# Performance work log

Measured on AMD Instinct MI355X. Metric: run time of the kernel, lower is better.

The kernel has to match this reference:

```python
import jax, jax.numpy as jnp
import numpy as np

D_MODEL = 1024
NUM_HEADS = 16
D_K = D_MODEL // NUM_HEADS


def setup_inputs() -> dict:
    key = jax.random.key(0)
    ks = jax.random.split(key, 9)
    B, S = 2, 2048
    scale = 1.0 / np.sqrt(D_MODEL)
    x = jax.random.normal(ks[0], (B, S, D_MODEL), dtype=jnp.float32)
    Wq = jax.random.normal(ks[1], (D_MODEL, D_MODEL), dtype=jnp.float32) * scale
    Wk = jax.random.normal(ks[2], (D_MODEL, D_MODEL), dtype=jnp.float32) * scale
    Wv = jax.random.normal(ks[3], (D_MODEL, D_MODEL), dtype=jnp.float32) * scale
    Wo = jax.random.normal(ks[4], (D_MODEL, D_MODEL), dtype=jnp.float32) * scale
    bq = jax.random.normal(ks[5], (D_MODEL,), dtype=jnp.float32) * 0.01
    bk = jax.random.normal(ks[6], (D_MODEL,), dtype=jnp.float32) * 0.01
    bv = jax.random.normal(ks[7], (D_MODEL,), dtype=jnp.float32) * 0.01
    bo = jax.random.normal(ks[8], (D_MODEL,), dtype=jnp.float32) * 0.01
    return {"x": x, "Wq": Wq, "bq": bq, "Wk": Wk, "bk": bk,
            "Wv": Wv, "bv": bv, "Wo": Wo, "bo": bo}


def reference(x, Wq, bq, Wk, bk, Wv, bv, Wo, bo):
    B, S, _ = x.shape
    H, Dk = NUM_HEADS, D_K
    # projections -> [B, H, S, Dk]
    def split_heads(t):
        return t.reshape(B, S, H, Dk).transpose(0, 2, 1, 3)
    q = split_heads(x @ Wq + bq)
    k = split_heads(x @ Wk + bk)
    v = split_heads(x @ Wv + bv)
    # full score matrix [B, H, S, S] (faithful to the original non-fused impl)
    scores = jnp.einsum('bhqd,bhkd->bhqk', q, k) / jnp.sqrt(jnp.float32(Dk))
    attn = jax.nn.softmax(scores, axis=-1)
    out = jnp.einsum('bhqk,bhkd->bhqd', attn, v)
    out = out.transpose(0, 2, 1, 3).reshape(B, S, H * Dk)
    return out @ Wo + bo
```

## Files before the change

### kernel.cpp

```cpp
#include <hip/hip_runtime.h>
#include <cstdint>

constexpr int S    = 2048;
constexpr int D    = 1024;
constexpr int NH   = 16;
constexpr int DK   = 64;
constexpr int MTOK = 2 * S;

typedef __bf16 bf16x8 __attribute__((ext_vector_type(8)));
typedef __bf16 bf16x4 __attribute__((ext_vector_type(4)));
typedef float  floatx4 __attribute__((ext_vector_type(4)));

__device__ __forceinline__ void async_cp16(const void* g, void* l) {
    __builtin_amdgcn_global_load_lds(
        (const __attribute__((address_space(1))) uint32_t*)g,
        (__attribute__((address_space(3))) uint32_t*)l, 16, 0, 0);
}

__global__ __launch_bounds__(256) void cvt_prep(
    const float* __restrict__ x, __bf16* __restrict__ xb,
    const float* __restrict__ W0, const float* __restrict__ W1,
    const float* __restrict__ W2, const float* __restrict__ W3,
    __bf16* __restrict__ T0, __bf16* __restrict__ T1,
    __bf16* __restrict__ T2, __bf16* __restrict__ T3)
{
    const int t = threadIdx.x;
    if (blockIdx.z == 4) {
        int blk = blockIdx.y * 16 + blockIdx.x;
        const float4* src = (const float4*)x;
        #pragma unroll
        for (int ii = 0; ii < 16; ++ii) {
            int idx = blk * 4096 + ii * 256 + t;
            float4 v = src[idx];
            bf16x4 o;
            o[0] = (__bf16)v.x; o[1] = (__bf16)v.y; o[2] = (__bf16)v.z; o[3] = (__bf16)v.w;
            *(bf16x4*)&xb[(size_t)idx * 4] = o;
        }
        return;
    }
    const float* W = (blockIdx.z == 0) ? W0 : (blockIdx.z == 1) ? W1 : (blockIdx.z == 2) ? W2 : W3;
    __bf16*      T = (blockIdx.z == 0) ? T0 : (blockIdx.z == 1) ? T1 : (blockIdx.z == 2) ? T2 : T3;
    __shared__ __bf16 tile[64][65];
    const int k0 = blockIdx.y * 64, n0 = blockIdx.x * 64;
    #pragma unroll
    for (int i = 0; i < 4; ++i) {
        int k = (t >> 4) + i * 16;
        int n = (t & 15) * 4;
        float4 v = *(const float4*)&W[(size_t)(k0 + k) * D + n0 + n];
        tile[n + 0][k] = (__bf16)v.x;
        tile[n + 1][k] = (__bf16)v.y;
        tile[n + 2][k] = (__bf16)v.z;
        tile[n + 3][k] = (__bf16)v.w;
    }
    __syncthreads();
    #pragma unroll
    for (int i = 0; i < 4; ++i) {
        int n = (t >> 4) + i * 16;
        int k = (t & 15) * 4;
        bf16x4 o;
        o[0] = tile[n][k]; o[1] = tile[n][k + 1]; o[2] = tile[n][k + 2]; o[3] = tile[n][k + 3];
        *(bf16x4*)&T[(size_t)(n0 + n) * D + k0 + k] = o;
    }
}

constexpr int BM = 128, BK = 64;

template<int JT>
__device__ __forceinline__ void gemm_core(
    const __bf16* __restrict__ A, const __bf16* __restrict__ Bt,
    __bf16* Alds, __bf16* Blds, int m0, int n0, floatx4 (&acc)[4][JT])
{
    const int tid = threadIdx.x;
    const int w = tid >> 6, l = tid & 63;
    const int wm = (w >> 1) * 64, wn = (w & 1) * 16 * JT;
    const int lr = l & 15, lg = l >> 4;

    #pragma unroll
    for (int i = 0; i < 4; ++i)
        #pragma unroll
        for (int j = 0; j < JT; ++j)
            acc[i][j] = (floatx4){0.f, 0.f, 0.f, 0.f};

    for (int k0 = 0; k0 < D; k0 += BK) {
        #pragma unroll
        for (int i = 0; i < 4; ++i) {
            int c = i * 256 + tid, row = c >> 3, g = c & 7;
            async_cp16(&A[(size_t)(m0 + row) * D + k0 + g * 8], &Alds[c * 8]);
        }
        #pragma unroll
        for (int i = 0; i < JT; ++i) {
            int c = i * 256 + tid, row = c >> 3, g = c & 7;
            async_cp16(&Bt[(size_t)(n0 + row) * D + k0 + g * 8], &Blds[c * 8]);
        }
        __syncthreads();
        #pragma unroll
        for (int kk = 0; kk < 2; ++kk) {
            bf16x8 af[4], bfr[JT];
            #pragma unroll
            for (int i = 0; i < 4; ++i)
                af[i] = *(const bf16x8*)&Alds[(wm + i * 16 + lr) * BK + kk * 32 + lg * 8];
            #pragma unroll
            for (int j = 0; j < JT; ++j)
                bfr[j] = *(const bf16x8*)&Blds[(wn + j * 16 + lr) * BK + kk * 32 + lg * 8];
            #pragma unroll
            for (int i = 0; i < 4; ++i)
                #pragma unroll
                for (int j = 0; j < JT; ++j)
                    acc[i][j] = __builtin_amdgcn_mfma_f32_16x16x32_bf16(af[i], bfr[j], acc[i][j], 0, 0, 0);
        }
        __syncthreads();
    }
}

__global__ __launch_bounds__(256, 2) void gemm_qkv(
    const __bf16* __restrict__ xb,
    const __bf16* __restrict__ WqT, const __bf16* __restrict__ WkT, const __bf16* __restrict__ WvT,
    const float* __restrict__ bq, const float* __restrict__ bk, const float* __restrict__ bv,
    __bf16* __restrict__ Qb, __bf16* __restrict__ Kb, __bf16* __restrict__ Vt)
{
    __shared__ __align__(16) __bf16 Alds[BM * BK];
    __shared__ __align__(16) __bf16 Blds[128 * BK];
    const int z = blockIdx.z;
    const __bf16* Bt   = (z == 0) ? WqT : (z == 1) ? WkT : WvT;
    const float*  bias = (z == 0) ? bq : (z == 1) ? bk : bv;
    const float   scale = (z == 0) ? 0.18033688f : 1.0f;
    const int m0 = blockIdx.y * BM, n0 = blockIdx.x * 128;

    floatx4 acc[4][4];
    gemm_core<4>(xb, Bt, Alds, Blds, m0, n0, acc);

    const int tid = threadIdx.x;
    const int w = tid >> 6, l = tid & 63;
    const int wm = (w >> 1) * 64, wn = (w & 1) * 64;
    const int lr = l & 15, lg = l >> 4;

    if (z < 2) {
        __bf16* Out = (z == 0) ? Qb : Kb;
        #pragma unroll
        for (int i = 0; i < 4; ++i)
            #pragma unroll
            for (int j = 0; j < 4; ++j) {
                int n = n0 + wn + j * 16 + lr;
                #pragma unroll
                for (int r = 0; r < 4; ++r) {
                    int m = m0 + wm + i * 16 + lg * 4 + r;
                    float v = (acc[i][j][r] + bias[n]) * scale;
                    size_t off = ((size_t)((m >> 11) * NH + (n >> 6)) * S + (m & (S - 1))) * DK + (n & (DK - 1));
                    Out[off] = (__bf16)v;
                }
            }
    } else {
        #pragma unroll
        for (int i = 0; i < 4; ++i)
            #pragma unroll
            for (int j = 0; j < 4; ++j) {
                int n = n0 + wn + j * 16 + lr;
                int m = m0 + wm + i * 16 + lg * 4;
                float bn = bias[n];
                bf16x4 o;
                #pragma unroll
                for (int r = 0; r < 4; ++r) o[r] = (__bf16)(acc[i][j][r] + bn);
                size_t off = ((size_t)((m >> 11) * NH + (n >> 6)) * DK + (n & (DK - 1))) * S + (m & (S - 1));
                *(bf16x4*)&Vt[off] = o;
            }
    }
}

__global__ __launch_bounds__(256, 2) void gemm_out(
    const __bf16* __restrict__ A, const __bf16* __restrict__ Bt,
    const float* __restrict__ bias, float* __restrict__ Cout)
{
    __shared__ __align__(16) __bf16 Alds[BM * BK];
    __shared__ __align__(16) __bf16 Blds[64 * BK];
    const int m0 = blockIdx.y * BM, n0 = blockIdx.x * 64;

    floatx4 acc[4][2];
    gemm_core<2>(A, Bt, Alds, Blds, m0, n0, acc);

    const int tid = threadIdx.x;
    const int w = tid >> 6, l = tid & 63;
    const int wm = (w >> 1) * 64, wn = (w & 1) * 32;
    const int lr = l & 15, lg = l >> 4;
    #pragma unroll
    for (int i = 0; i < 4; ++i)
        #pragma unroll
        for (int j = 0; j < 2; ++j) {
            int n = n0 + wn + j * 16 + lr;
            #pragma unroll
            for (int r = 0; r < 4; ++r) {
                int m = m0 + wm + i * 16 + lg * 4 + r;
                Cout[(size_t)m * D + n] = acc[i][j][r] + bias[n];
            }
        }
}

constexpr int QT = 128;
constexpr int KT = 64;
constexpr float SOFTMAX_C2 = 14.4269504f;

__global__ __launch_bounds__(256, 2) void attn_mfma(
    const __bf16* __restrict__ Q, const __bf16* __restrict__ K,
    const __bf16* __restrict__ Vt, __bf16* __restrict__ O)
{
    __shared__ __align__(16) __bf16 Klds[2][KT * DK];
    __shared__ __align__(16) __bf16 Vlds[2][DK * KT];
    __shared__ __align__(16) __bf16 Plds[4][32 * 64];

    const int tid = threadIdx.x;
    const int w = tid >> 6, l = tid & 63;
    const int lr = l & 15, lg = l >> 4;
    const int sw = lr & 7;
    const int bh = blockIdx.y;
    const int q0 = blockIdx.x * QT;
    const __bf16* Kbase = K  + (size_t)bh * S * DK;
    const __bf16* Vbase = Vt + (size_t)bh * DK * S;

    bf16x8 qf[2][2];
    {
        const __bf16* qp = Q + ((size_t)bh * S + q0 + w * 32) * DK;
        #pragma unroll
        for (int i = 0; i < 2; ++i)
            #pragma unroll
            for (int kk = 0; kk < 2; ++kk)
                qf[i][kk] = *(const bf16x8*)&qp[(i * 16 + lr) * DK + kk * 32 + lg * 8];
    }
    bf16x8 vones;
    #pragma unroll
    for (int j = 0; j < 8; ++j) vones[j] = (__bf16)1.0f;

    floatx4 acc[4][2];
    #pragma unroll
    for (int jd = 0; jd < 4; ++jd)
        #pragma unroll
        for (int i = 0; i < 2; ++i)
            acc[jd][i] = (floatx4){0.f, 0.f, 0.f, 0.f};
    floatx4 psacc[2];
    psacc[0] = (floatx4){0.f, 0.f, 0.f, 0.f};
    psacc[1] = (floatx4){0.f, 0.f, 0.f, 0.f};

    bf16x8 kreg[2], vreg[2];
    auto gload = [&](int t0) {
        #pragma unroll
        for (int ii = 0; ii < 2; ++ii) {
            int c = ii * 256 + tid, row = c >> 3, g = c & 7;
            kreg[ii] = *(const bf16x8*)&Kbase[(size_t)(t0 + row) * DK + g * 8];
            vreg[ii] = *(const bf16x8*)&Vbase[(size_t)row * S + t0 + g * 8];
        }
    };
    auto lwrite = [&](int buf) {
        #pragma unroll
        for (int ii = 0; ii < 2; ++ii) {
            int c = ii * 256 + tid, row = c >> 3, gs = (c & 7) ^ (row & 7);
            *(bf16x8*)&Klds[buf][row * 64 + gs * 8] = kreg[ii];
            *(bf16x8*)&Vlds[buf][row * 64 + gs * 8] = vreg[ii];
        }
    };

    gload(0);
    lwrite(0);
    gload(KT);

    for (int t0 = 0; t0 < S; t0 += KT) {
        const int cur = (t0 >> 6) & 1;
        __syncthreads();

        floatx4 sa[4][2];
        #pragma unroll
        for (int j = 0; j < 4; ++j)
            #pragma unroll
            for (int i = 0; i < 2; ++i)
                sa[j][i] = (floatx4){0.f, 0.f, 0.f, 0.f};
        #pragma unroll
        for (int kk = 0; kk < 2; ++kk) {
            bf16x8 kf[4];
            #pragma unroll
            for (int j = 0; j < 4; ++j)
                kf[j] = *(const bf16x8*)&Klds[cur][(j * 16 + lr) * DK + (((kk * 4 + lg) ^ sw) * 8)];
            #pragma unroll
            for (int j = 0; j < 4; ++j)
                #pragma unroll
                for (int i = 0; i < 2; ++i)
                    sa[j][i] = __builtin_amdgcn_mfma_f32_16x16x32_bf16(kf[j], qf[i][kk], sa[j][i], 0, 0, 0);
        }

        #pragma unroll
        for (int j = 0; j < 4; ++j)
            #pragma unroll
            for (int i = 0; i < 2; ++i) {
                bf16x4 pb;
                #pragma unroll
                for (int r = 0; r < 4; ++r)
                    pb[r] = (__bf16)__builtin_amdgcn_exp2f(sa[j][i][r] - SOFTMAX_C2);
                int gsw = (j * 2 + (lg >> 1)) ^ sw;
                *(bf16x4*)&Plds[w][(i * 16 + lr) * 64 + gsw * 8 + (lg & 1) * 4] = pb;
            }

        #pragma unroll
        for (int kk = 0; kk < 2; ++kk) {
            bf16x8 vf[4], pf[2];
            #pragma unroll
            for (int i = 0; i < 2; ++i) {
                int gsw = (kk * 4 + lg) ^ sw;
                pf[i] = *(const bf16x8*)&Plds[w][(i * 16 + lr) * 64 + gsw * 8];
            }
            #pragma unroll
            for (int jd = 0; jd < 4; ++jd)
                vf[jd] = *(const bf16x8*)&Vlds[cur][(jd * 16 + lr) * KT + (((kk * 4 + lg) ^ sw) * 8)];
            #pragma unroll
            for (int jd = 0; jd < 4; ++jd)
                #pragma unroll
                for (int i = 0; i < 2; ++i)
                    acc[jd][i] = __builtin_amdgcn_mfma_f32_16x16x32_bf16(vf[jd], pf[i], acc[jd][i], 0, 0, 0);
            #pragma unroll
            for (int i = 0; i < 2; ++i)
                psacc[i] = __builtin_amdgcn_mfma_f32_16x16x32_bf16(vones, pf[i], psacc[i], 0, 0, 0);
        }

        if (t0 + KT < S) {
            lwrite(cur ^ 1);
            if (t0 + 2 * KT < S) gload(t0 + 2 * KT);
        }
    }

    const int b = bh >> 4, h = bh & 15;
    #pragma unroll
    for (int i = 0; i < 2; ++i) {
        float inv = 1.f / psacc[i][0];
        int q = q0 + w * 32 + i * 16 + lr;
        __bf16* op = O + (size_t)(b * S + q) * D + h * DK;
        #pragma unroll
        for (int jd = 0; jd < 4; ++jd) {
            bf16x4 ov;
            #pragma unroll
            for (int r = 0; r < 4; ++r) ov[r] = (__bf16)(acc[jd][i][r] * inv);
            *(bf16x4*)&op[jd * 16 + lg * 4] = ov;
        }
    }
}

extern "C" void kernel_launch(void* const* d_in, const int* in_sizes, int n_in,
                              void* d_out, int out_size, void* d_ws, size_t ws_size,
                              hipStream_t stream) {
    const float* x  = (const float*)d_in[0];
    const float* Wq = (const float*)d_in[1];
    const float* bq = (const float*)d_in[2];
    const float* Wk = (const float*)d_in[3];
    const float* bk = (const float*)d_in[4];
    const float* Wv = (const float*)d_in[5];
    const float* bv = (const float*)d_in[6];
    const float* Wo = (const float*)d_in[7];
    const float* bo = (const float*)d_in[8];

    char* ws = (char*)d_ws;
    __bf16* xb  = (__bf16*)(ws);
    __bf16* WqT = (__bf16*)(ws + (8ull  << 20));
    __bf16* WkT = (__bf16*)(ws + (10ull << 20));
    __bf16* WvT = (__bf16*)(ws + (12ull << 20));
    __bf16* WoT = (__bf16*)(ws + (14ull << 20));
    __bf16* Qb  = (__bf16*)(ws + (16ull << 20));
    __bf16* Kb  = (__bf16*)(ws + (24ull << 20));
    __bf16* Vt  = (__bf16*)(ws + (32ull << 20));
    __bf16* Ob  = (__bf16*)(ws + (40ull << 20));

    cvt_prep<<<dim3(16, 16, 5), 256, 0, stream>>>(
        x, xb, Wq, Wk, Wv, Wo, WqT, WkT, WvT, WoT);

    gemm_qkv<<<dim3(D / 128, MTOK / BM, 3), 256, 0, stream>>>(
        xb, WqT, WkT, WvT, bq, bk, bv, Qb, Kb, Vt);

    attn_mfma<<<dim3(S / QT, 2 * NH), 256, 0, stream>>>(Qb, Kb, Vt, Ob);

    gemm_out<<<dim3(D / 64, MTOK / BM), 256, 0, stream>>>(Ob, WoT, bo, (float*)d_out);
}
```

Measured before the change: 190.7 us.

## Pre-swizzle K/V in projection epilogue and stream tiles via async global-to-LDS copies

The QKV projection epilogue now writes K and V^T in a tile-blocked, XOR-swizzled layout that matches the attention kernel's LDS layout. The attention kernel can then copy each 64-row tile straight into LDS with global_load_lds, instead of staging it through registers and writing it to LDS. This frees registers and drops the explicit LDS store instructions. The diff also folds the softmax constant into the score accumulator's initial value and raises wave priority around the MFMA sections. The trade-offs are scattered 2-byte stores in the K epilogue and a full vmcnt(0) wait at the end of every iteration, which limits prefetch depth to one tile.

```diff
diff --git a/kernel.cpp b/kernel.cpp
--- a/kernel.cpp
+++ b/kernel.cpp
@@ -123,7 +123,6 @@
     const int z = blockIdx.z;
     const __bf16* Bt   = (z == 0) ? WqT : (z == 1) ? WkT : WvT;
     const float*  bias = (z == 0) ? bq : (z == 1) ? bk : bv;
-    const float   scale = (z == 0) ? 0.18033688f : 1.0f;
     const int m0 = blockIdx.y * BM, n0 = blockIdx.x * 128;
 
     floatx4 acc[4][4];
@@ -134,8 +133,8 @@
     const int wm = (w >> 1) * 64, wn = (w & 1) * 64;
     const int lr = l & 15, lg = l >> 4;
 
-    if (z < 2) {
-        __bf16* Out = (z == 0) ? Qb : Kb;
+    if (z == 0) {
+        const float scale = 0.18033688f;
         #pragma unroll
         for (int i = 0; i < 4; ++i)
             #pragma unroll
@@ -146,21 +145,43 @@
                     int m = m0 + wm + i * 16 + lg * 4 + r;
                     float v = (acc[i][j][r] + bias[n]) * scale;
                     size_t off = ((size_t)((m >> 11) * NH + (n >> 6)) * S + (m & (S - 1))) * DK + (n & (DK - 1));
-                    Out[off] = (__bf16)v;
+                    Qb[off] = (__bf16)v;
                 }
             }
-    } else {
+    } else if (z == 1) {
         #pragma unroll
         for (int i = 0; i < 4; ++i)
             #pragma unroll
             for (int j = 0; j < 4; ++j) {
                 int n = n0 + wn + j * 16 + lr;
+                int dk = n & 63;
+                float bn = bias[n];
+                #pragma unroll
+                for (int r = 0; r < 4; ++r) {
+                    int m = m0 + wm + i * 16 + lg * 4 + r;
+                    int s = m & (S - 1);
+                    int bhh = (m >> 11) * NH + (n >> 6);
+                    size_t off = (size_t)bhh * S * DK + (size_t)(s >> 6) * 4096
+                               + (s & 63) * 64 + (((dk >> 3) ^ (s & 7)) * 8) + (dk & 7);
+                    Kb[off] = (__bf16)(acc[i][j][r] + bn);
+                }
+            }
+    } else {
+        #pragma unroll
+        for (int i = 0; i < 4; ++i)
+            #pragma unroll
+            for (int j = 0; j < 4; ++j) {
+                int n = n0 + wn + j * 16 + lr;
+                int dk = n & 63;
                 int m = m0 + wm + i * 16 + lg * 4;
+                int s = m & (S - 1);
+                int bhh = (m >> 11) * NH + (n >> 6);
                 float bn = bias[n];
                 bf16x4 o;
                 #pragma unroll
                 for (int r = 0; r < 4; ++r) o[r] = (__bf16)(acc[i][j][r] + bn);
-                size_t off = ((size_t)((m >> 11) * NH + (n >> 6)) * DK + (n & (DK - 1))) * S + (m & (S - 1));
+                size_t off = (size_t)bhh * DK * S + (size_t)(s >> 6) * 4096
+                           + dk * 64 + ((((s >> 3) & 7) ^ (dk & 7)) * 8) + (s & 7);
                 *(bf16x4*)&Vt[off] = o;
             }
     }
@@ -199,8 +220,8 @@
 constexpr float SOFTMAX_C2 = 14.4269504f;
 
 __global__ __launch_bounds__(256, 2) void attn_mfma(
-    const __bf16* __restrict__ Q, const __bf16* __restrict__ K,
-    const __bf16* __restrict__ Vt, __bf16* __restrict__ O)
+    const __bf16* __restrict__ Q, const __bf16* __restrict__ Kswz,
+    const __bf16* __restrict__ Vswz, __bf16* __restrict__ O)
 {
     __shared__ __align__(16) __bf16 Klds[2][KT * DK];
     __shared__ __align__(16) __bf16 Vlds[2][DK * KT];
@@ -212,8 +233,8 @@
     const int sw = lr & 7;
     const int bh = blockIdx.y;
     const int q0 = blockIdx.x * QT;
-    const __bf16* Kbase = K  + (size_t)bh * S * DK;
-    const __bf16* Vbase = Vt + (size_t)bh * DK * S;
+    const __bf16* Kb = Kswz + (size_t)bh * S * DK;
+    const __bf16* Vb = Vswz + (size_t)bh * DK * S;
 
     bf16x8 qf[2][2];
     {
@@ -238,38 +259,33 @@
     psacc[0] = (floatx4){0.f, 0.f, 0.f, 0.f};
     psacc[1] = (floatx4){0.f, 0.f, 0.f, 0.f};
 
-    bf16x8 kreg[2], vreg[2];
-    auto gload = [&](int t0) {
+    auto issue = [&](int tile, int buf) {
+        const __bf16* ks = Kb + (size_t)tile * 4096;
+        const __bf16* vs = Vb + (size_t)tile * 4096;
         #pragma unroll
         for (int ii = 0; ii < 2; ++ii) {
-            int c = ii * 256 + tid, row = c >> 3, g = c & 7;
-            kreg[ii] = *(const bf16x8*)&Kbase[(size_t)(t0 + row) * DK + g * 8];
-            vreg[ii] = *(const bf16x8*)&Vbase[(size_t)row * S + t0 + g * 8];
+            int c = ii * 256 + tid;
+            async_cp16(&ks[c * 8], &Klds[buf][c * 8]);
+            async_cp16(&vs[c * 8], &Vlds[buf][c * 8]);
         }
     };
-    auto lwrite = [&](int buf) {
-        #pragma unroll
-        for (int ii = 0; ii < 2; ++ii) {
-            int c = ii * 256 + tid, row = c >> 3, gs = (c & 7) ^ (row & 7);
-            *(bf16x8*)&Klds[buf][row * 64 + gs * 8] = kreg[ii];
-            *(bf16x8*)&Vlds[buf][row * 64 + gs * 8] = vreg[ii];
-        }
-    };
-
-    gload(0);
-    lwrite(0);
-    gload(KT);
+
+    issue(0, 0);
+    asm volatile("s_waitcnt vmcnt(0)" ::: "memory");
 
     for (int t0 = 0; t0 < S; t0 += KT) {
-        const int cur = (t0 >> 6) & 1;
+        const int tt = t0 >> 6;
+        const int cur = tt & 1;
         __syncthreads();
+        if (t0 + KT < S) issue(tt + 1, cur ^ 1);
 
         floatx4 sa[4][2];
         #pragma unroll
         for (int j = 0; j < 4; ++j)
             #pragma unroll
             for (int i = 0; i < 2; ++i)
-                sa[j][i] = (floatx4){0.f, 0.f, 0.f, 0.f};
+                sa[j][i] = (floatx4){-SOFTMAX_C2, -SOFTMAX_C2, -SOFTMAX_C2, -SOFTMAX_C2};
+        __builtin_amdgcn_s_setprio(1);
         #pragma unroll
         for (int kk = 0; kk < 2; ++kk) {
             bf16x8 kf[4];
@@ -282,6 +298,7 @@
                 for (int i = 0; i < 2; ++i)
                     sa[j][i] = __builtin_amdgcn_mfma_f32_16x16x32_bf16(kf[j], qf[i][kk], sa[j][i], 0, 0, 0);
         }
+        __builtin_amdgcn_s_setprio(0);
 
         #pragma unroll
         for (int j = 0; j < 4; ++j)
@@ -290,11 +307,12 @@
                 bf16x4 pb;
                 #pragma unroll
                 for (int r = 0; r < 4; ++r)
-                    pb[r] = (__bf16)__builtin_amdgcn_exp2f(sa[j][i][r] - SOFTMAX_C2);
+                    pb[r] = (__bf16)__builtin_amdgcn_exp2f(sa[j][i][r]);
                 int gsw = (j * 2 + (lg >> 1)) ^ sw;
                 *(bf16x4*)&Plds[w][(i * 16 + lr) * 64 + gsw * 8 + (lg & 1) * 4] = pb;
             }
 
+        __builtin_amdgcn_s_setprio(1);
         #pragma unroll
         for (int kk = 0; kk < 2; ++kk) {
             bf16x8 vf[4], pf[2];
@@ -315,11 +333,9 @@
             for (int i = 0; i < 2; ++i)
                 psacc[i] = __builtin_amdgcn_mfma_f32_16x16x32_bf16(vones, pf[i], psacc[i], 0, 0, 0);
         }
-
-        if (t0 + KT < S) {
-            lwrite(cur ^ 1);
-            if (t0 + 2 * KT < S) gload(t0 + 2 * KT);
-        }
+        __builtin_amdgcn_s_setprio(0);
+
+        asm volatile("s_waitcnt vmcnt(0)" ::: "memory");
     }
 
     const int b = bh >> 4, h = bh & 15;
```

Measured after the change: 191.2 us. Within noise of the previous version (+0.2%).
